# Kernel optimization log

Measured on AMD Instinct MI355X. Metric: run time of the kernel, lower is better.

Reference implementation:

```python
import jax, jax.numpy as jnp
import numpy as np


def setup_inputs() -> dict:
    key = jax.random.key(0)
    k1, k2, k3 = jax.random.split(key, 3)
    shape = (32, 64, 128, 128)  # B, C, H, W
    out = jax.random.normal(k1, shape, dtype=jnp.float32)
    vals = jax.random.normal(k2, shape, dtype=jnp.float32)
    keep = jax.random.uniform(k3, shape) < 0.1
    target = jnp.where(keep, vals, 0.0).astype(jnp.float32)
    return {"out": out, "target": target}


def reference(out, target):
    # Original loops over every nonzero index of target and sums
    # F.smooth_l1_loss (beta=1, mean over a single scalar == elementwise value).
    # Equivalent fused form: masked elementwise smooth-L1, summed.
    d = jnp.abs(out - target)
    sl1 = jnp.where(d < 1.0, 0.5 * d * d, d - 0.5)
    mask = target != 0.0
    return jnp.sum(jnp.where(mask, sl1, 0.0))
```

## Files before the change

kernel.cpp:

```cpp
#include <hip/hip_runtime.h>


typedef float v4f __attribute__((ext_vector_type(4)));

__device__ __forceinline__ float sl1_masked(float o, float t) {
    float d = fabsf(o - t);
    float s = (d < 1.0f) ? (0.5f * d * d) : (d - 0.5f);
    return (t != 0.0f) ? s : 0.0f;
}

__device__ __forceinline__ float sl1_v4(v4f o, v4f t) {
    return sl1_masked(o.x, t.x) + sl1_masked(o.y, t.y) +
           sl1_masked(o.z, t.z) + sl1_masked(o.w, t.w);
}

__device__ __forceinline__ float block_reduce(float acc) {
    #pragma unroll
    for (int off = 32; off > 0; off >>= 1)
        acc += __shfl_down(acc, off, 64);
    __shared__ float wave_sums[4];
    const int lane = threadIdx.x & 63;
    const int wave = threadIdx.x >> 6;
    if (lane == 0) wave_sums[wave] = acc;
    __syncthreads();
    return wave_sums[0] + wave_sums[1] + wave_sums[2] + wave_sums[3];
}

__global__ __launch_bounds__(256) void sl1_partial_kernel(
    const v4f* __restrict__ o4,
    const v4f* __restrict__ t4,
    float* __restrict__ partials,
    long long n4)
{
    const long long stride = (long long)gridDim.x * blockDim.x;
    long long i = (long long)blockIdx.x * blockDim.x + threadIdx.x;

    float acc = 0.0f;
    if (i < n4) {
        v4f o_cur = __builtin_nontemporal_load(&o4[i]);
        v4f t_cur = __builtin_nontemporal_load(&t4[i]);
        for (long long j = i + stride; j < n4; j += stride) {
            v4f o_nxt = __builtin_nontemporal_load(&o4[j]);
            v4f t_nxt = __builtin_nontemporal_load(&t4[j]);
            acc += sl1_v4(o_cur, t_cur);
            o_cur = o_nxt;
            t_cur = t_nxt;
        }
        acc += sl1_v4(o_cur, t_cur);
    }

    float s = block_reduce(acc);
    if (threadIdx.x == 0) partials[blockIdx.x] = s;
}

__global__ __launch_bounds__(256) void sl1_final_kernel(
    const float* __restrict__ partials,
    float* __restrict__ result,
    int n)
{
    float acc = 0.0f;
    for (int i = threadIdx.x; i < n; i += 256)
        acc += partials[i];
    float s = block_reduce(acc);
    if (threadIdx.x == 0) result[0] = s;
}

extern "C" void kernel_launch(void* const* d_in, const int* in_sizes, int n_in,
                              void* d_out, int out_size, void* d_ws, size_t ws_size,
                              hipStream_t stream) {
    const v4f* o4 = (const v4f*)d_in[0];
    const v4f* t4 = (const v4f*)d_in[1];
    float* res      = (float*)d_out;
    float* partials = (float*)d_ws;

    const long long n  = (long long)in_sizes[0];
    const long long n4 = n / 4;

    const int block = 256;
    const int grid  = 4096;

    sl1_partial_kernel<<<grid, block, 0, stream>>>(o4, t4, partials, n4);
    sl1_final_kernel<<<1, block, 0, stream>>>(partials, res, grid);
}
```

Measured before the change: 254.6 us.

## Replace grid-stride loop with fixed-chunk blocks and 4-deep load prefetch

```diff
diff --git a/kernel.cpp b/kernel.cpp
--- a/kernel.cpp
+++ b/kernel.cpp
@@ -2,6 +2,10 @@
 
 
 typedef float v4f __attribute__((ext_vector_type(4)));
+
+#define ITERS 16
+#define BLOCK 256
+#define CHUNK (BLOCK * ITERS)
 
 __device__ __forceinline__ float sl1_masked(float o, float t) {
     float d = fabsf(o - t);
@@ -18,7 +22,7 @@
     #pragma unroll
     for (int off = 32; off > 0; off >>= 1)
         acc += __shfl_down(acc, off, 64);
-    __shared__ float wave_sums[4];
+    __shared__ float wave_sums[BLOCK / 64];
     const int lane = threadIdx.x & 63;
     const int wave = threadIdx.x >> 6;
     if (lane == 0) wave_sums[wave] = acc;
@@ -26,40 +30,54 @@
     return wave_sums[0] + wave_sums[1] + wave_sums[2] + wave_sums[3];
 }
 
-__global__ __launch_bounds__(256) void sl1_partial_kernel(
+__global__ __launch_bounds__(BLOCK) void sl1_partial_kernel(
     const v4f* __restrict__ o4,
     const v4f* __restrict__ t4,
     float* __restrict__ partials,
     long long n4)
 {
-    const long long stride = (long long)gridDim.x * blockDim.x;
-    long long i = (long long)blockIdx.x * blockDim.x + threadIdx.x;
+    const long long base = (long long)blockIdx.x * CHUNK + threadIdx.x;
+    float acc = 0.0f;
 
-    float acc = 0.0f;
-    if (i < n4) {
-        v4f o_cur = __builtin_nontemporal_load(&o4[i]);
-        v4f t_cur = __builtin_nontemporal_load(&t4[i]);
-        for (long long j = i + stride; j < n4; j += stride) {
-            v4f o_nxt = __builtin_nontemporal_load(&o4[j]);
-            v4f t_nxt = __builtin_nontemporal_load(&t4[j]);
-            acc += sl1_v4(o_cur, t_cur);
-            o_cur = o_nxt;
-            t_cur = t_nxt;
+    if (base + (ITERS - 1) * BLOCK < n4) {
+        v4f o[4], t[4];
+        #pragma unroll
+        for (int k = 0; k < 4; ++k) {
+            o[k] = __builtin_nontemporal_load(&o4[base + k * BLOCK]);
+            t[k] = __builtin_nontemporal_load(&t4[base + k * BLOCK]);
         }
-        acc += sl1_v4(o_cur, t_cur);
+        #pragma unroll
+        for (int k = 0; k < ITERS; ++k) {
+            const int s = k & 3;
+            acc += sl1_v4(o[s], t[s]);
+            if (k + 4 < ITERS) {
+                o[s] = __builtin_nontemporal_load(&o4[base + (k + 4) * BLOCK]);
+                t[s] = __builtin_nontemporal_load(&t4[base + (k + 4) * BLOCK]);
+            }
+        }
+    } else {
+        #pragma unroll
+        for (int k = 0; k < ITERS; ++k) {
+            long long idx = base + (long long)k * BLOCK;
+            if (idx < n4) {
+                v4f o = __builtin_nontemporal_load(&o4[idx]);
+                v4f t = __builtin_nontemporal_load(&t4[idx]);
+                acc += sl1_v4(o, t);
+            }
+        }
     }
 
     float s = block_reduce(acc);
     if (threadIdx.x == 0) partials[blockIdx.x] = s;
 }
 
-__global__ __launch_bounds__(256) void sl1_final_kernel(
+__global__ __launch_bounds__(BLOCK) void sl1_final_kernel(
     const float* __restrict__ partials,
     float* __restrict__ result,
     int n)
 {
     float acc = 0.0f;
-    for (int i = threadIdx.x; i < n; i += 256)
+    for (int i = threadIdx.x; i < n; i += BLOCK)
         acc += partials[i];
     float s = block_reduce(acc);
     if (threadIdx.x == 0) result[0] = s;
@@ -76,9 +94,7 @@
     const long long n  = (long long)in_sizes[0];
     const long long n4 = n / 4;
 
-    const int block = 256;
-    const int grid  = 4096;
-
-    sl1_partial_kernel<<<grid, block, 0, stream>>>(o4, t4, partials, n4);
-    sl1_final_kernel<<<1, block, 0, stream>>>(partials, res, grid);
+    const int grid = (int)((n4 + CHUNK - 1) / CHUNK);
+    sl1_partial_kernel<<<grid, BLOCK, 0, stream>>>(o4, t4, partials, n4);
+    sl1_final_kernel<<<1, BLOCK, 0, stream>>>(partials, res, grid);
 }
```

New measurement: 249.7 us. No clear change (-1.9%).
